# Performance work log

Hardware: AMD Instinct MI355X
Metric: run time of the kernel (lower is better)

Reference implementation:

```python
import jax, jax.numpy as jnp
import numpy as np

# AF2 IPA dims
N, CS, CZ, E, PQ, PV, H = 768, 384, 128, 16, 4, 8, 12
SCALE_SINGLE = 1.0 / np.sqrt(E)
SCALE_FRAME = -1.0 / np.sqrt(18.0 * PQ)


def setup_inputs() -> dict:
    key = jax.random.key(0)
    ks = jax.random.split(key, 14)
    single = jax.random.normal(ks[0], (N, CS), jnp.float32)
    pair = jax.random.normal(ks[1], (N, N, CZ), jnp.float32)
    R, _ = jnp.linalg.qr(jax.random.normal(ks[2], (N, 3, 3), jnp.float32))  # proper per-residue rotations
    t = jax.random.normal(ks[3], (N, 3), jnp.float32)

    def w(k, shape):
        return jax.random.normal(k, shape, jnp.float32) / np.sqrt(shape[0])

    Wq = w(ks[4], (CS, H * E))
    Wk = w(ks[5], (CS, H * E))
    Wv = w(ks[6], (CS, H * E))
    Wqp = w(ks[7], (CS, H * PQ * 3))
    Wkp = w(ks[8], (CS, H * PQ * 3))
    Wvp = w(ks[9], (CS, H * PV * 3))
    Wb = w(ks[10], (CZ, H))
    D_out = H * (CZ + E + PV * 4)  # 2112
    Wout = w(ks[11], (D_out, CS))
    bout = jnp.zeros((CS,), jnp.float32)
    scale_head = jnp.ones((H,), jnp.float32)
    return dict(single_representation=single, pair_representation=pair,
                frame_rotations=R, frame_translations=t,
                Wq=Wq, Wk=Wk, Wv=Wv, Wqp=Wqp, Wkp=Wkp, Wvp=Wvp,
                Wb=Wb, Wout=Wout, bout=bout, scale_head=scale_head)


def reference(single_representation, pair_representation, frame_rotations, frame_translations,
              Wq, Wk, Wv, Wqp, Wkp, Wvp, Wb, Wout, bout, scale_head):
    s, z, R, t = single_representation, pair_representation, frame_rotations, frame_translations
    # --- attention weights from three sources ---
    q = (s @ Wq).reshape(N, H, E)
    k = (s @ Wk).reshape(N, H, E)
    v = (s @ Wv).reshape(N, H, E)
    w_single = SCALE_SINGLE * jnp.einsum('ihe,jhe->hij', q, k)  # [H,N,N]
    w_pair = (z @ Wb).transpose(2, 0, 1)                        # [H,N,N]

    qp = (s @ Wqp).reshape(N, H, PQ, 3)
    kp = (s @ Wkp).reshape(N, H, PQ, 3)
    # Frame.apply: x_global = R_n x + t_n
    gq = jnp.einsum('nab,nhpb->nhpa', R, qp) + t[:, None, None, :]
    gk = jnp.einsum('nab,nhpb->nhpa', R, kp) + t[:, None, None, :]
    # sum_p ||gq_i^hp - gk_j^hp||^2 expanded to avoid [N,N,H,P,3] intermediate
    sq_q = jnp.sum(gq * gq, axis=(-1, -2)).T   # [H,N]
    sq_k = jnp.sum(gk * gk, axis=(-1, -2)).T   # [H,N]
    dot = jnp.einsum('ihpc,jhpc->hij', gq, gk)
    d2 = sq_q[:, :, None] + sq_k[:, None, :] - 2.0 * dot  # [H,N,N]
    w_frame = SCALE_FRAME * jax.nn.softplus(scale_head)[:, None, None] * d2

    a = jax.nn.softmax(w_single + w_pair + w_frame, axis=-1)  # [H,N,N]

    # --- three value paths ---
    o_s = jnp.einsum('hij,jhe->ihe', a, v).reshape(N, H * E)
    o_z = jnp.einsum('hij,ijc->ihc', a, z).reshape(N, H * CZ)

    vp = (s @ Wvp).reshape(N, H, PV, 3)
    gv = jnp.einsum('nab,nhpb->nhpa', R, vp) + t[:, None, None, :]
    so = jnp.einsum('hij,jhpc->ihpc', a, gv)                    # [N,H,PV,3] in global frame
    # Frame.inverse applied: R_i^T (x - t_i)
    local = jnp.einsum('nba,nhpb->nhpa', R, so - t[:, None, None, :])
    pts = local.transpose(0, 2, 1, 3).reshape(N, PV * H * 3)    # (point, head, xyz) flatten
    norms = jnp.linalg.norm(local, axis=-1).transpose(0, 2, 1).reshape(N, PV * H)

    att = jnp.concatenate([o_s, o_z, pts, norms], axis=-1)      # [N, H*(E+CZ+4*PV)]
    return att @ Wout + bout
```

## Files before the change

kernel.cpp:

```cpp
#include <hip/hip_runtime.h>
#include <hip/hip_bf16.h>

#define NN 768
#define CSD 384
#define CZD 128
#define HD 12
#define DOUT 2112
#define II 2

#define SCALE_SINGLE 0.25f
#define SCALE_FRAME (-0.11785113019775793f)

__device__ __forceinline__ float dot4f(float4 a, float4 b){
    return fmaf(a.x,b.x, fmaf(a.y,b.y, fmaf(a.z,b.z, a.w*b.w)));
}

__global__ __launch_bounds__(384) void k_proj(
    const float* __restrict__ s, const float* __restrict__ R, const float* __restrict__ tv,
    const float* __restrict__ Wq, const float* __restrict__ Wk, const float* __restrict__ Wv,
    const float* __restrict__ Wqp, const float* __restrict__ Wkp, const float* __restrict__ Wvp,
    float* __restrict__ q, float* __restrict__ k, float* __restrict__ v,
    float* __restrict__ gq, float* __restrict__ gk, float* __restrict__ gv,
    float* __restrict__ sqq, float* __restrict__ sqk)
{
    __shared__ float s_l[II*CSD];
    __shared__ float praw[II][576];
    __shared__ float sq_pt[II][96];
    int i0 = blockIdx.x * II, t = threadIdx.x;
    if (t < II*CSD/4){
        const float4* s4 = (const float4*)(s + (size_t)i0*CSD);
        ((float4*)s_l)[t] = s4[t];
    }
    __syncthreads();

    int cols[3] = {t, t+384, t+768};
    const float* Wp[3]; int st[3], lc[3];
    #pragma unroll
    for (int m=0;m<3;m++){
        int c = cols[m];
        if (c < 192){ Wp[m]=Wq;  st[m]=192; lc[m]=c; }
        else if (c < 384){ Wp[m]=Wk;  st[m]=192; lc[m]=c-192; }
        else if (c < 576){ Wp[m]=Wv;  st[m]=192; lc[m]=c-384; }
        else if (c < 720){ Wp[m]=Wqp; st[m]=144; lc[m]=c-576; }
        else if (c < 864){ Wp[m]=Wkp; st[m]=144; lc[m]=c-720; }
        else { Wp[m]=Wvp; st[m]=288; lc[m]=c-864; }
    }
    float acc[3][II];
    #pragma unroll
    for (int m=0;m<3;m++)
        #pragma unroll
        for (int ii=0;ii<II;ii++) acc[m][ii]=0.f;

    #pragma unroll 4
    for (int r=0;r<CSD;r++){
        float w0 = Wp[0][(size_t)r*st[0]+lc[0]];
        float w1 = Wp[1][(size_t)r*st[1]+lc[1]];
        float w2 = Wp[2][(size_t)r*st[2]+lc[2]];
        #pragma unroll
        for (int ii=0;ii<II;ii++){
            float sv = s_l[ii*CSD + r];
            acc[0][ii] = fmaf(sv, w0, acc[0][ii]);
            acc[1][ii] = fmaf(sv, w1, acc[1][ii]);
            acc[2][ii] = fmaf(sv, w2, acc[2][ii]);
        }
    }
    #pragma unroll
    for (int m=0;m<3;m++){
        int c = cols[m];
        #pragma unroll
        for (int ii=0;ii<II;ii++){
            float val = acc[m][ii];
            size_t i = i0 + ii;
            if (c < 192) q[i*192 + c] = val;
            else if (c < 384) k[i*192 + (c-192)] = val;
            else if (c < 576) v[i*192 + (c-384)] = val;
            else praw[ii][c-576] = val;
        }
    }
    __syncthreads();

    if (t < 192){
        #pragma unroll
        for (int ii=0;ii<II;ii++){
            size_t i = i0 + ii;
            const float* Ri = R + i*9;
            float R00=Ri[0],R01=Ri[1],R02=Ri[2];
            float R10=Ri[3],R11=Ri[4],R12=Ri[5];
            float R20=Ri[6],R21=Ri[7],R22=Ri[8];
            float t0=tv[i*3+0],t1=tv[i*3+1],t2=tv[i*3+2];
            int src; float* dst; int sqslot=-1;
            if (t < 48){ src = t*3; dst = gq + i*144 + t*3; sqslot = t; }
            else if (t < 96){ int u=t-48; src = 144+u*3; dst = gk + i*144 + u*3; sqslot = 48+u; }
            else { int u=t-96; src = 288+u*3; dst = gv + i*288 + u*3; }
            float x=praw[ii][src], y=praw[ii][src+1], zc=praw[ii][src+2];
            float g0 = fmaf(R00,x, fmaf(R01,y, fmaf(R02,zc, t0)));
            float g1 = fmaf(R10,x, fmaf(R11,y, fmaf(R12,zc, t1)));
            float g2 = fmaf(R20,x, fmaf(R21,y, fmaf(R22,zc, t2)));
            dst[0]=g0; dst[1]=g1; dst[2]=g2;
            if (sqslot >= 0) sq_pt[ii][sqslot] = g0*g0 + g1*g1 + g2*g2;
        }
    }
    __syncthreads();
    if (t < II*HD){
        int ii = t / HD, h = t % HD;
        float s1 = sq_pt[ii][h*4]+sq_pt[ii][h*4+1]+sq_pt[ii][h*4+2]+sq_pt[ii][h*4+3];
        float s2 = sq_pt[ii][48+h*4]+sq_pt[ii][48+h*4+1]+sq_pt[ii][48+h*4+2]+sq_pt[ii][48+h*4+3];
        sqq[(size_t)(i0+ii)*HD + h] = s1;
        sqk[(size_t)(i0+ii)*HD + h] = s2;
    }
}

__global__ __launch_bounds__(512) void k_ipa(
    const float* __restrict__ z, const float* __restrict__ Wb, const float* __restrict__ scale_head,
    const float* __restrict__ q, const float* __restrict__ k,
    const float* __restrict__ gq, const float* __restrict__ gk,
    const float* __restrict__ sqq, const float* __restrict__ sqk,
    const float* __restrict__ v, const float* __restrict__ gv,
    const float* __restrict__ R, const float* __restrict__ tv,
    float* __restrict__ att)
{
    __shared__ float ztile[4][32][CZD];
    __shared__ float wbT[HD*CZD];
    __shared__ float qloc[360];
    __shared__ float a_l[HD][NN];
    __shared__ float so_l[288];

    int i = blockIdx.x, t = threadIdx.x;
    int wave = t >> 6, lane = t & 63;
    int r = lane & 31, half = lane >> 5;

    for (int idx=t; idx<HD*CZD; idx+=512){
        int h = idx >> 7, c = idx & 127;
        wbT[idx] = Wb[(size_t)c*HD + h];
    }
    if (t < 192) qloc[t] = q[(size_t)i*192 + t];
    else if (t < 336) qloc[t] = gq[(size_t)i*144 + (t-192)];
    else if (t < 348) qloc[t] = sqq[(size_t)i*HD + (t-336)];
    else if (t < 360){
        int h = t-348;
        float shv = scale_head[h];
        float sp = (shv > 20.f) ? shv : log1pf(__expf(shv));
        qloc[t] = SCALE_FRAME * sp;
    }

    const char* zi = (const char*)(z + (size_t)i*NN*CZD);
    float* zbase = &ztile[0][0][0];

#define WAITV(N) asm volatile("s_waitcnt vmcnt(" #N ")" ::: "memory")
#define BARX() do{ asm volatile("" ::: "memory"); __builtin_amdgcn_s_barrier(); asm volatile("" ::: "memory"); }while(0)

#define STAGEA(JT, BUF) do { \
    const char* _zb = zi + (size_t)(JT)*16384; \
    char* _lb = (char*)zbase + (size_t)(BUF)*16384; \
    _Pragma("unroll") \
    for (int _m=0;_m<4;_m++){ \
        int _d = t*16 + _m*4096; \
        int _j = _d >> 9; \
        int _b = _d & 511; \
        int _sb = _b ^ ((_j & 31) << 4); \
        __builtin_amdgcn_global_load_lds((const __attribute__((address_space(1))) void*)(_zb + (size_t)_j*512 + _sb), \
            (__attribute__((address_space(3))) void*)(_lb + _d), 16, 0, 0); \
    } \
  } while(0)

#define STAGEB(JT, BUF) do { \
    const char* _zb = zi + (size_t)(JT)*16384; \
    char* _lb = (char*)zbase + (size_t)(BUF)*16384; \
    _Pragma("unroll") \
    for (int _m=0;_m<4;_m++){ \
        int _d = t*16 + _m*4096; \
        __builtin_amdgcn_global_load_lds((const __attribute__((address_space(1))) void*)(_zb + _d), \
            (__attribute__((address_space(3))) void*)(_lb + _d), 16, 0, 0); \
    } \
  } while(0)

    __syncthreads();

    if (t < 256){ STAGEA(0,0); STAGEA(1,1); STAGEA(2,2); }

    float pairL[24];
    float SF[24][3];
    const float4* wb4 = (const float4*)wbT;
    const float4* qv4 = (const float4*)qloc;
    const float4* gq4 = (const float4*)(qloc + 192);
    int hpair = wave*2 + half;
    int gsing = (wave-6)*2 + half;
    int xoff = r << 4;

    #pragma unroll
    for (int jt=0; jt<24; ++jt){
        if (t < 256){
            if (jt < 22) WAITV(8);
            else if (jt == 22) WAITV(4);
            else WAITV(0);
        }
        BARX();
        if (t < 256 && jt+3 < 24) STAGEA(jt+3, (jt+3)&3);
        if (wave < 6){
            const char* zb = (const char*)zbase + (size_t)(jt&3)*16384 + (size_t)r*512;
            float p = 0.f;
            #pragma unroll 8
            for (int c4=0; c4<32; ++c4){
                float4 zv = *(const float4*)(zb + ((c4*16) ^ xoff));
                p += dot4f(zv, wb4[hpair*32 + c4]);
            }
            pairL[jt] = p;
        } else {
            int jg = jt*32 + r;
            const float4* kp  = (const float4*)(k  + (size_t)jg*192);
            const float4* gkp = (const float4*)(gk + (size_t)jg*144);
            #pragma unroll
            for (int hs=0; hs<3; ++hs){
                int h = gsing*3 + hs;
                float sng = dot4f(qv4[h*4+0], kp[h*4+0]) + dot4f(qv4[h*4+1], kp[h*4+1])
                          + dot4f(qv4[h*4+2], kp[h*4+2]) + dot4f(qv4[h*4+3], kp[h*4+3]);
                float fdot = dot4f(gq4[h*3+0], gkp[h*3+0]) + dot4f(gq4[h*3+1], gkp[h*3+1])
                           + dot4f(gq4[h*3+2], gkp[h*3+2]);
                float d2 = qloc[336+h] + sqk[(size_t)jg*HD + h] - 2.0f*fdot;
                SF[jt][hs] = fmaf(SCALE_SINGLE, sng, qloc[348+h]*d2);
            }
        }
    }
    __syncthreads();

    float* S_l = zbase;
    if (wave >= 6){
        #pragma unroll
        for (int jt=0; jt<24; ++jt){
            int b = (jt*32 + r)*13 + gsing*3;
            S_l[b+0] = SF[jt][0];
            S_l[b+1] = SF[jt][1];
            S_l[b+2] = SF[jt][2];
        }
    }
    __syncthreads();
    if (wave < 6){
        #pragma unroll
        for (int jt=0; jt<24; ++jt) pairL[jt] += S_l[(jt*32 + r)*13 + hpair];
        float m = -1e30f;
        #pragma unroll
        for (int jt=0; jt<24; ++jt) m = fmaxf(m, pairL[jt]);
        #pragma unroll
        for (int off=16; off; off>>=1) m = fmaxf(m, __shfl_xor(m, off));
        float ssum = 0.f;
        #pragma unroll
        for (int jt=0; jt<24; ++jt){ float e = __expf(pairL[jt]-m); pairL[jt]=e; ssum += e; }
        #pragma unroll
        for (int off=16; off; off>>=1) ssum += __shfl_xor(ssum, off);
        float inv = 1.0f/ssum;
        #pragma unroll
        for (int jt=0; jt<24; ++jt) a_l[hpair][jt*32 + r] = pairL[jt]*inv;
    }
    __syncthreads();

    if (t < 256){ STAGEB(0,0); STAGEB(1,1); STAGEB(2,2); }

    int hs2 = 0;
    const float4* gsrc = nullptr;
    int gstride = 0;
    if (t < 384){ hs2 = t>>5; }
    else if (t < 432){ int u=t-384; hs2 = u>>2; gsrc = (const float4*)v  + hs2*4 + (u&3); gstride = 48; }
    else if (t < 504){ int u=t-432; hs2 = u/6;  gsrc = (const float4*)gv + hs2*6 + (u%6); gstride = 72; }
    float4 acc = {0.f,0.f,0.f,0.f};
    int c4 = t & 31;

    for (int jt=0; jt<24; ++jt){
        if (t < 256){
            if (jt < 22) WAITV(8);
            else if (jt == 22) WAITV(4);
            else WAITV(0);
        }
        BARX();
        if (t < 256 && jt+3 < 24) STAGEB(jt+3, (jt+3)&3);
        if (t < 384){
            const float4* arow4 = (const float4*)&a_l[hs2][0];
            float4 af[8];
            #pragma unroll
            for (int m=0;m<8;m++) af[m] = arow4[jt*8 + m];
            const float4* zt4 = (const float4*)(zbase + (size_t)(jt&3)*4096);
            #pragma unroll
            for (int jj=0;jj<32;jj++){
                float aw = ((const float*)af)[jj];
                float4 zv = zt4[jj*32 + c4];
                acc.x = fmaf(aw, zv.x, acc.x);
                acc.y = fmaf(aw, zv.y, acc.y);
                acc.z = fmaf(aw, zv.z, acc.z);
                acc.w = fmaf(aw, zv.w, acc.w);
            }
        } else if (t < 504){
            const float* arow = &a_l[hs2][0];
            #pragma unroll
            for (int jj=0;jj<32;jj++){
                int j = jt*32 + jj;
                float aw = arow[j];
                float4 sv = gsrc[(size_t)j*gstride];
                acc.x = fmaf(aw, sv.x, acc.x);
                acc.y = fmaf(aw, sv.y, acc.y);
                acc.z = fmaf(aw, sv.z, acc.z);
                acc.w = fmaf(aw, sv.w, acc.w);
            }
        }
    }

    if (t < 384){
        float4* dst = (float4*)(att + (size_t)i*DOUT + 192) + (hs2*32 + c4);
        *dst = acc;
    } else if (t < 432){
        int u = t-384;
        float4* dst = (float4*)(att + (size_t)i*DOUT) + u;
        *dst = acc;
    } else if (t < 504){
        int u = t-432;
        ((float4*)so_l)[u] = acc;
    }
    __syncthreads();
    if (t < 96){
        int h = t >> 3, p = t & 7;
        float d0 = so_l[h*24+p*3+0] - tv[(size_t)i*3+0];
        float d1 = so_l[h*24+p*3+1] - tv[(size_t)i*3+1];
        float d2 = so_l[h*24+p*3+2] - tv[(size_t)i*3+2];
        const float* Ri = R + (size_t)i*9;
        float l0 = fmaf(Ri[0],d0, fmaf(Ri[3],d1, Ri[6]*d2));
        float l1 = fmaf(Ri[1],d0, fmaf(Ri[4],d1, Ri[7]*d2));
        float l2 = fmaf(Ri[2],d0, fmaf(Ri[5],d1, Ri[8]*d2));
        size_t base = (size_t)i*DOUT;
        att[base + 1728 + p*36 + h*3 + 0] = l0;
        att[base + 1728 + p*36 + h*3 + 1] = l1;
        att[base + 1728 + p*36 + h*3 + 2] = l2;
        att[base + 2016 + p*12 + h] = sqrtf(l0*l0 + l1*l1 + l2*l2);
    }
#undef STAGEA
#undef STAGEB
#undef WAITV
#undef BARX
}

#define ROWS4 2
__global__ __launch_bounds__(384) void k_final(
    const float* __restrict__ att, const float* __restrict__ Wout, const float* __restrict__ bout,
    float* __restrict__ out)
{
    __shared__ float att_l[ROWS4*DOUT];
    int ib = blockIdx.x * ROWS4, t = threadIdx.x;
    for (int idx=t; idx<ROWS4*DOUT; idx+=384){
        att_l[idx] = att[(size_t)ib*DOUT + idx];
    }
    __syncthreads();
    float a0=0.f,a1=0.f,a2=0.f,a3=0.f;
    float b0=0.f,b1=0.f,b2=0.f,b3=0.f;
    #pragma unroll 4
    for (int d=0; d<DOUT; d+=4){
        float w0 = Wout[(size_t)(d+0)*CSD + t];
        float w1 = Wout[(size_t)(d+1)*CSD + t];
        float w2 = Wout[(size_t)(d+2)*CSD + t];
        float w3 = Wout[(size_t)(d+3)*CSD + t];
        a0 = fmaf(att_l[d+0], w0, a0);
        a1 = fmaf(att_l[d+1], w1, a1);
        a2 = fmaf(att_l[d+2], w2, a2);
        a3 = fmaf(att_l[d+3], w3, a3);
        b0 = fmaf(att_l[DOUT+d+0], w0, b0);
        b1 = fmaf(att_l[DOUT+d+1], w1, b1);
        b2 = fmaf(att_l[DOUT+d+2], w2, b2);
        b3 = fmaf(att_l[DOUT+d+3], w3, b3);
    }
    float bb = bout[t];
    out[(size_t)ib*CSD + t]     = bb + ((a0+a1)+(a2+a3));
    out[(size_t)(ib+1)*CSD + t] = bb + ((b0+b1)+(b2+b3));
}

extern "C" void kernel_launch(void* const* d_in, const int* in_sizes, int n_in,
                              void* d_out, int out_size, void* d_ws, size_t ws_size,
                              hipStream_t stream)
{
    const float* s   = (const float*)d_in[0];
    const float* z   = (const float*)d_in[1];
    const float* R   = (const float*)d_in[2];
    const float* tv  = (const float*)d_in[3];
    const float* Wq  = (const float*)d_in[4];
    const float* Wk  = (const float*)d_in[5];
    const float* Wv  = (const float*)d_in[6];
    const float* Wqp = (const float*)d_in[7];
    const float* Wkp = (const float*)d_in[8];
    const float* Wvp = (const float*)d_in[9];
    const float* Wb  = (const float*)d_in[10];
    const float* Wout= (const float*)d_in[11];
    const float* bout= (const float*)d_in[12];
    const float* sh  = (const float*)d_in[13];

    float* ws  = (float*)d_ws;
    float* q_  = ws;
    float* k_  = q_  + 147456;
    float* v_  = k_  + 147456;
    float* gq_ = v_  + 147456;
    float* gk_ = gq_ + 110592;
    float* gv_ = gk_ + 110592;
    float* sqq_= gv_ + 221184;
    float* sqk_= sqq_ + 9216;
    float* att_= sqk_ + 9216;
    float* out = (float*)d_out;

    hipLaunchKernelGGL(k_proj,  dim3(NN/II), dim3(384), 0, stream,
                       s,R,tv,Wq,Wk,Wv,Wqp,Wkp,Wvp, q_,k_,v_,gq_,gk_,gv_,sqq_,sqk_);
    hipLaunchKernelGGL(k_ipa,   dim3(NN),    dim3(512), 0, stream,
                       z,Wb,sh,q_,k_,gq_,gk_,sqq_,sqk_, v_,gv_,R,tv, att_);
    hipLaunchKernelGGL(k_final, dim3(NN/ROWS4), dim3(384), 0, stream,
                       att_,Wout,bout, out);
}
```

Measured before the change: 478.0 us.

## Rebalance IPA kernel waves: register-blocked pair bias and o_z, dedicated staging waves

Restructures the per-row IPA kernel's work split. Wave 0 now computes all 12 pair-bias logits with 2x3 register blocking. Waves 6-7 add the single/frame logits into a padded a_l buffer one tile late, which removes the SF register array and the S_l shuffle. Softmax is redone as a full-wave float4 pass over a_l. The o_z accumulation moves to two waves, each computing 3 heads per z load, while waves 2-5 only issue z staging loads. The goal is fewer redundant LDS reads of z and less register pressure, at the risk of concentrating compute on fewer waves and serializing work behind barriers.

```diff
diff --git a/kernel.cpp b/kernel.cpp
--- a/kernel.cpp
+++ b/kernel.cpp
@@ -7,6 +7,8 @@
 #define HD 12
 #define DOUT 2112
 #define II 2
+#define ALS 772
+#define WBS 132
 
 #define SCALE_SINGLE 0.25f
 #define SCALE_FRAME (-0.11785113019775793f)
@@ -120,41 +122,32 @@
     float* __restrict__ att)
 {
     __shared__ float ztile[4][32][CZD];
-    __shared__ float wbT[HD*CZD];
-    __shared__ float qloc[360];
-    __shared__ float a_l[HD][NN];
+    __shared__ float wbT[HD*WBS];
+    __shared__ float a_l[HD*ALS];
     __shared__ float so_l[288];
 
     int i = blockIdx.x, t = threadIdx.x;
     int wave = t >> 6, lane = t & 63;
-    int r = lane & 31, half = lane >> 5;
+    bool stg = (t >= 128 && t < 384);
+    int ts = t - 128;
 
     for (int idx=t; idx<HD*CZD; idx+=512){
         int h = idx >> 7, c = idx & 127;
-        wbT[idx] = Wb[(size_t)c*HD + h];
-    }
-    if (t < 192) qloc[t] = q[(size_t)i*192 + t];
-    else if (t < 336) qloc[t] = gq[(size_t)i*144 + (t-192)];
-    else if (t < 348) qloc[t] = sqq[(size_t)i*HD + (t-336)];
-    else if (t < 360){
-        int h = t-348;
-        float shv = scale_head[h];
-        float sp = (shv > 20.f) ? shv : log1pf(__expf(shv));
-        qloc[t] = SCALE_FRAME * sp;
+        wbT[h*WBS + c] = Wb[(size_t)c*HD + h];
     }
 
     const char* zi = (const char*)(z + (size_t)i*NN*CZD);
     float* zbase = &ztile[0][0][0];
 
 #define WAITV(N) asm volatile("s_waitcnt vmcnt(" #N ")" ::: "memory")
-#define BARX() do{ asm volatile("" ::: "memory"); __builtin_amdgcn_s_barrier(); asm volatile("" ::: "memory"); }while(0)
+#define BARX() do{ asm volatile("s_waitcnt lgkmcnt(0)" ::: "memory"); __builtin_amdgcn_s_barrier(); asm volatile("" ::: "memory"); }while(0)
 
 #define STAGEA(JT, BUF) do { \
     const char* _zb = zi + (size_t)(JT)*16384; \
     char* _lb = (char*)zbase + (size_t)(BUF)*16384; \
     _Pragma("unroll") \
     for (int _m=0;_m<4;_m++){ \
-        int _d = t*16 + _m*4096; \
+        int _d = ts*16 + _m*4096; \
         int _j = _d >> 9; \
         int _b = _d & 511; \
         int _sb = _b ^ ((_j & 31) << 4); \
@@ -168,150 +161,197 @@
     char* _lb = (char*)zbase + (size_t)(BUF)*16384; \
     _Pragma("unroll") \
     for (int _m=0;_m<4;_m++){ \
-        int _d = t*16 + _m*4096; \
+        int _d = ts*16 + _m*4096; \
         __builtin_amdgcn_global_load_lds((const __attribute__((address_space(1))) void*)(_zb + _d), \
             (__attribute__((address_space(3))) void*)(_lb + _d), 16, 0, 0); \
     } \
   } while(0)
 
-    __syncthreads();
-
-    if (t < 256){ STAGEA(0,0); STAGEA(1,1); STAGEA(2,2); }
-
-    float pairL[24];
-    float SF[24][3];
-    const float4* wb4 = (const float4*)wbT;
-    const float4* qv4 = (const float4*)qloc;
-    const float4* gq4 = (const float4*)(qloc + 192);
-    int hpair = wave*2 + half;
-    int gsing = (wave-6)*2 + half;
-    int xoff = r << 4;
-
-    #pragma unroll
+    int rgrp = lane & 15, gp = lane >> 4;
+    int rS = lane & 31, gS = (wave-6)*2 + (lane>>5);
+    float4 qv[3][4]; float4 gqv[3][3]; float sqq3[3], sp3[3];
+    if (wave >= 6){
+        #pragma unroll
+        for (int hs=0; hs<3; ++hs){
+            int h = gS*3 + hs;
+            const float4* qp = (const float4*)(q + (size_t)i*192 + h*16);
+            qv[hs][0]=qp[0]; qv[hs][1]=qp[1]; qv[hs][2]=qp[2]; qv[hs][3]=qp[3];
+            const float4* gp4 = (const float4*)(gq + (size_t)i*144 + h*12);
+            gqv[hs][0]=gp4[0]; gqv[hs][1]=gp4[1]; gqv[hs][2]=gp4[2];
+            sqq3[hs] = sqq[(size_t)i*HD + h];
+            float shv = scale_head[h];
+            float sp = (shv > 20.f) ? shv : log1pf(__expf(shv));
+            sp3[hs] = SCALE_FRAME * sp;
+        }
+    }
+
+    __syncthreads();
+    if (stg){ STAGEA(0,0); STAGEA(1,1); STAGEA(2,2); }
+
+    float SFp0=0.f, SFp1=0.f, SFp2=0.f;
+
     for (int jt=0; jt<24; ++jt){
-        if (t < 256){
+        if (stg){
             if (jt < 22) WAITV(8);
             else if (jt == 22) WAITV(4);
             else WAITV(0);
         }
         BARX();
-        if (t < 256 && jt+3 < 24) STAGEA(jt+3, (jt+3)&3);
-        if (wave < 6){
-            const char* zb = (const char*)zbase + (size_t)(jt&3)*16384 + (size_t)r*512;
-            float p = 0.f;
+        if (stg && jt+3 < 24) STAGEA(jt+3, (jt+3)&3);
+        if (wave == 0){
+            const char* zrow0 = (const char*)zbase + (size_t)(jt&3)*16384 + (size_t)rgrp*512;
+            const char* zrow1 = zrow0 + 16*512;
+            int x0 = rgrp<<4, x1 = (rgrp+16)<<4;
+            const float4* wbg = (const float4*)(wbT + gp*3*WBS);
+            float L00=0.f,L01=0.f,L02=0.f,L10=0.f,L11=0.f,L12=0.f;
             #pragma unroll 8
             for (int c4=0; c4<32; ++c4){
-                float4 zv = *(const float4*)(zb + ((c4*16) ^ xoff));
-                p += dot4f(zv, wb4[hpair*32 + c4]);
-            }
-            pairL[jt] = p;
-        } else {
-            int jg = jt*32 + r;
+                float4 z0 = *(const float4*)(zrow0 + ((c4*16) ^ x0));
+                float4 z1 = *(const float4*)(zrow1 + ((c4*16) ^ x1));
+                float4 w0 = wbg[c4];
+                float4 w1 = wbg[33 + c4];
+                float4 w2 = wbg[66 + c4];
+                L00 += dot4f(z0,w0); L01 += dot4f(z0,w1); L02 += dot4f(z0,w2);
+                L10 += dot4f(z1,w0); L11 += dot4f(z1,w1); L12 += dot4f(z1,w2);
+            }
+            int j0 = jt*32 + rgrp;
+            a_l[(gp*3+0)*ALS + j0] = L00;  a_l[(gp*3+0)*ALS + j0+16] = L10;
+            a_l[(gp*3+1)*ALS + j0] = L01;  a_l[(gp*3+1)*ALS + j0+16] = L11;
+            a_l[(gp*3+2)*ALS + j0] = L02;  a_l[(gp*3+2)*ALS + j0+16] = L12;
+        } else if (wave >= 6){
+            if (jt > 0){
+                int jp = (jt-1)*32 + rS;
+                a_l[(gS*3+0)*ALS + jp] += SFp0;
+                a_l[(gS*3+1)*ALS + jp] += SFp1;
+                a_l[(gS*3+2)*ALS + jp] += SFp2;
+            }
+            int jg = jt*32 + rS;
             const float4* kp  = (const float4*)(k  + (size_t)jg*192);
             const float4* gkp = (const float4*)(gk + (size_t)jg*144);
+            float sf[3];
             #pragma unroll
             for (int hs=0; hs<3; ++hs){
-                int h = gsing*3 + hs;
-                float sng = dot4f(qv4[h*4+0], kp[h*4+0]) + dot4f(qv4[h*4+1], kp[h*4+1])
-                          + dot4f(qv4[h*4+2], kp[h*4+2]) + dot4f(qv4[h*4+3], kp[h*4+3]);
-                float fdot = dot4f(gq4[h*3+0], gkp[h*3+0]) + dot4f(gq4[h*3+1], gkp[h*3+1])
-                           + dot4f(gq4[h*3+2], gkp[h*3+2]);
-                float d2 = qloc[336+h] + sqk[(size_t)jg*HD + h] - 2.0f*fdot;
-                SF[jt][hs] = fmaf(SCALE_SINGLE, sng, qloc[348+h]*d2);
-            }
-        }
-    }
-    __syncthreads();
-
-    float* S_l = zbase;
+                int h = gS*3 + hs;
+                float sng = dot4f(qv[hs][0], kp[h*4+0]) + dot4f(qv[hs][1], kp[h*4+1])
+                          + dot4f(qv[hs][2], kp[h*4+2]) + dot4f(qv[hs][3], kp[h*4+3]);
+                float fdot = dot4f(gqv[hs][0], gkp[h*3+0]) + dot4f(gqv[hs][1], gkp[h*3+1])
+                           + dot4f(gqv[hs][2], gkp[h*3+2]);
+                float d2 = sqq3[hs] + sqk[(size_t)jg*HD + h] - 2.0f*fdot;
+                sf[hs] = fmaf(SCALE_SINGLE, sng, sp3[hs]*d2);
+            }
+            SFp0 = sf[0]; SFp1 = sf[1]; SFp2 = sf[2];
+        }
+    }
+    BARX();
     if (wave >= 6){
-        #pragma unroll
-        for (int jt=0; jt<24; ++jt){
-            int b = (jt*32 + r)*13 + gsing*3;
-            S_l[b+0] = SF[jt][0];
-            S_l[b+1] = SF[jt][1];
-            S_l[b+2] = SF[jt][2];
-        }
-    }
-    __syncthreads();
+        int jp = 23*32 + rS;
+        a_l[(gS*3+0)*ALS + jp] += SFp0;
+        a_l[(gS*3+1)*ALS + jp] += SFp1;
+        a_l[(gS*3+2)*ALS + jp] += SFp2;
+    }
+    __syncthreads();
+
     if (wave < 6){
         #pragma unroll
-        for (int jt=0; jt<24; ++jt) pairL[jt] += S_l[(jt*32 + r)*13 + hpair];
-        float m = -1e30f;
-        #pragma unroll
-        for (int jt=0; jt<24; ++jt) m = fmaxf(m, pairL[jt]);
-        #pragma unroll
-        for (int off=16; off; off>>=1) m = fmaxf(m, __shfl_xor(m, off));
-        float ssum = 0.f;
-        #pragma unroll
-        for (int jt=0; jt<24; ++jt){ float e = __expf(pairL[jt]-m); pairL[jt]=e; ssum += e; }
-        #pragma unroll
-        for (int off=16; off; off>>=1) ssum += __shfl_xor(ssum, off);
-        float inv = 1.0f/ssum;
-        #pragma unroll
-        for (int jt=0; jt<24; ++jt) a_l[hpair][jt*32 + r] = pairL[jt]*inv;
-    }
-    __syncthreads();
-
-    if (t < 256){ STAGEB(0,0); STAGEB(1,1); STAGEB(2,2); }
-
-    int hs2 = 0;
-    const float4* gsrc = nullptr;
-    int gstride = 0;
-    if (t < 384){ hs2 = t>>5; }
-    else if (t < 432){ int u=t-384; hs2 = u>>2; gsrc = (const float4*)v  + hs2*4 + (u&3); gstride = 48; }
-    else if (t < 504){ int u=t-432; hs2 = u/6;  gsrc = (const float4*)gv + hs2*6 + (u%6); gstride = 72; }
-    float4 acc = {0.f,0.f,0.f,0.f};
-    int c4 = t & 31;
+        for (int hh=0; hh<2; ++hh){
+            int h = wave*2 + hh;
+            float4* row4 = (float4*)(a_l + h*ALS);
+            float4 vls[3];
+            #pragma unroll
+            for (int qq=0; qq<3; ++qq) vls[qq] = row4[lane + 64*qq];
+            float m = -1e30f;
+            #pragma unroll
+            for (int qq=0; qq<3; ++qq){
+                m = fmaxf(m, fmaxf(fmaxf(vls[qq].x, vls[qq].y), fmaxf(vls[qq].z, vls[qq].w)));
+            }
+            #pragma unroll
+            for (int off=32; off; off>>=1) m = fmaxf(m, __shfl_xor(m, off));
+            float ssum = 0.f;
+            #pragma unroll
+            for (int qq=0; qq<3; ++qq){
+                vls[qq].x = __expf(vls[qq].x - m); vls[qq].y = __expf(vls[qq].y - m);
+                vls[qq].z = __expf(vls[qq].z - m); vls[qq].w = __expf(vls[qq].w - m);
+                ssum += (vls[qq].x + vls[qq].y) + (vls[qq].z + vls[qq].w);
+            }
+            #pragma unroll
+            for (int off=32; off; off>>=1) ssum += __shfl_xor(ssum, off);
+            float inv = 1.0f/ssum;
+            #pragma unroll
+            for (int qq=0; qq<3; ++qq){
+                vls[qq].x *= inv; vls[qq].y *= inv; vls[qq].z *= inv; vls[qq].w *= inv;
+                row4[lane + 64*qq] = vls[qq];
+            }
+        }
+    }
+    __syncthreads();
+
+    if (stg){ STAGEB(0,0); STAGEB(1,1); STAGEB(2,2); }
+
+    int c4 = lane & 31;
+    int hgz = wave*2 + (lane>>5);
+    float4 az0={0,0,0,0}, az1={0,0,0,0}, az2={0,0,0,0};
+    float4 accs = {0,0,0,0};
+    const float4* gsrc = nullptr; int gstride = 0; int hso = 0;
+    if (t >= 384 && t < 432){ int u=t-384; hso = u>>2; gsrc = (const float4*)v  + hso*4 + (u&3); gstride = 48; }
+    else if (t >= 432 && t < 504){ int u=t-432; hso = u/6;  gsrc = (const float4*)gv + hso*6 + (u%6); gstride = 72; }
 
     for (int jt=0; jt<24; ++jt){
-        if (t < 256){
+        if (stg){
             if (jt < 22) WAITV(8);
             else if (jt == 22) WAITV(4);
             else WAITV(0);
         }
         BARX();
-        if (t < 256 && jt+3 < 24) STAGEB(jt+3, (jt+3)&3);
-        if (t < 384){
-            const float4* arow4 = (const float4*)&a_l[hs2][0];
-            float4 af[8];
-            #pragma unroll
-            for (int m=0;m<8;m++) af[m] = arow4[jt*8 + m];
+        if (stg && jt+3 < 24) STAGEB(jt+3, (jt+3)&3);
+        if (wave < 2){
             const float4* zt4 = (const float4*)(zbase + (size_t)(jt&3)*4096);
-            #pragma unroll
-            for (int jj=0;jj<32;jj++){
-                float aw = ((const float*)af)[jj];
-                float4 zv = zt4[jj*32 + c4];
-                acc.x = fmaf(aw, zv.x, acc.x);
-                acc.y = fmaf(aw, zv.y, acc.y);
-                acc.z = fmaf(aw, zv.z, acc.z);
-                acc.w = fmaf(aw, zv.w, acc.w);
-            }
-        } else if (t < 504){
-            const float* arow = &a_l[hs2][0];
-            #pragma unroll
-            for (int jj=0;jj<32;jj++){
+            const float4* arow = (const float4*)a_l;
+            int h0 = hgz*3;
+            #pragma unroll
+            for (int jq=0; jq<8; ++jq){
+                float4 a0 = arow[(h0+0)*(ALS/4) + jt*8 + jq];
+                float4 a1 = arow[(h0+1)*(ALS/4) + jt*8 + jq];
+                float4 a2 = arow[(h0+2)*(ALS/4) + jt*8 + jq];
+                #pragma unroll
+                for (int u=0; u<4; ++u){
+                    float4 zv = zt4[(jq*4+u)*32 + c4];
+                    float w0 = ((const float*)&a0)[u];
+                    float w1 = ((const float*)&a1)[u];
+                    float w2 = ((const float*)&a2)[u];
+                    az0.x = fmaf(w0, zv.x, az0.x); az0.y = fmaf(w0, zv.y, az0.y);
+                    az0.z = fmaf(w0, zv.z, az0.z); az0.w = fmaf(w0, zv.w, az0.w);
+                    az1.x = fmaf(w1, zv.x, az1.x); az1.y = fmaf(w1, zv.y, az1.y);
+                    az1.z = fmaf(w1, zv.z, az1.z); az1.w = fmaf(w1, zv.w, az1.w);
+                    az2.x = fmaf(w2, zv.x, az2.x); az2.y = fmaf(w2, zv.y, az2.y);
+                    az2.z = fmaf(w2, zv.z, az2.z); az2.w = fmaf(w2, zv.w, az2.w);
+                }
+            }
+        } else if (t >= 384 && t < 504){
+            const float* arow = a_l + hso*ALS;
+            #pragma unroll
+            for (int jj=0; jj<32; ++jj){
                 int j = jt*32 + jj;
                 float aw = arow[j];
                 float4 sv = gsrc[(size_t)j*gstride];
-                acc.x = fmaf(aw, sv.x, acc.x);
-                acc.y = fmaf(aw, sv.y, acc.y);
-                acc.z = fmaf(aw, sv.z, acc.z);
-                acc.w = fmaf(aw, sv.w, acc.w);
-            }
-        }
-    }
-
-    if (t < 384){
-        float4* dst = (float4*)(att + (size_t)i*DOUT + 192) + (hs2*32 + c4);
-        *dst = acc;
-    } else if (t < 432){
+                accs.x = fmaf(aw, sv.x, accs.x);
+                accs.y = fmaf(aw, sv.y, accs.y);
+                accs.z = fmaf(aw, sv.z, accs.z);
+                accs.w = fmaf(aw, sv.w, accs.w);
+            }
+        }
+    }
+
+    if (wave < 2){
+        int h0 = hgz*3;
+        *(float4*)(att + (size_t)i*DOUT + 192 + (h0+0)*128 + c4*4) = az0;
+        *(float4*)(att + (size_t)i*DOUT + 192 + (h0+1)*128 + c4*4) = az1;
+        *(float4*)(att + (size_t)i*DOUT + 192 + (h0+2)*128 + c4*4) = az2;
+    } else if (t >= 384 && t < 432){
         int u = t-384;
-        float4* dst = (float4*)(att + (size_t)i*DOUT) + u;
-        *dst = acc;
-    } else if (t < 504){
+        ((float4*)(att + (size_t)i*DOUT))[u] = accs;
+    } else if (t >= 432 && t < 504){
         int u = t-432;
-        ((float4*)so_l)[u] = acc;
+        ((float4*)so_l)[u] = accs;
     }
     __syncthreads();
     if (t < 96){
```

New measurement: 576.7 us. 1.21x slower.
